# Kernel optimization log

Measured on AMD Instinct MI355X. Metric: run time of the kernel, lower is better.

The kernel has to match this reference:

```python
import jax, jax.numpy as jnp
import numpy as np

B, L, E, D, H, P, NL = 4, 2048, 7, 512, 8, 720, 2
DH = D // H
FACTOR = 5
U = min(L, FACTOR * int(np.ceil(np.log(L))))  # top-u queries, = 40
SCALE = 1.0 / np.sqrt(DH)


def setup_inputs() -> dict:
    key = jax.random.key(0)
    ks = jax.random.split(key, 12)
    s = 0.02
    rn = lambda k, shape: jax.random.normal(k, shape, jnp.float32) * s
    return {
        "x": jax.random.normal(ks[0], (B, L, E), jnp.float32),
        "emb_w": rn(ks[1], (E, D)), "emb_b": jnp.zeros((D,), jnp.float32),
        "Wq": rn(ks[2], (NL, D, D)), "bq": jnp.zeros((NL, D), jnp.float32),
        "Wk": rn(ks[3], (NL, D, D)), "bk": jnp.zeros((NL, D), jnp.float32),
        "Wv": rn(ks[4], (NL, D, D)), "bv": jnp.zeros((NL, D), jnp.float32),
        "Wo": rn(ks[5], (NL, D, D)), "bo": jnp.zeros((NL, D), jnp.float32),
        "W1": rn(ks[6], (NL, D, D)), "b1": jnp.zeros((NL, D), jnp.float32),
        "W2": rn(ks[7], (NL, D, D)), "b2": jnp.zeros((NL, D), jnp.float32),
        "ln1_g": jnp.ones((NL, D), jnp.float32), "ln1_b": jnp.zeros((NL, D), jnp.float32),
        "ln2_g": jnp.ones((NL, D), jnp.float32), "ln2_b": jnp.zeros((NL, D), jnp.float32),
        "proj_w": rn(ks[8], (D, E)), "proj_b": jnp.zeros((E,), jnp.float32),
    }


def layer_norm(x, g, b):
    m = jnp.mean(x, axis=-1, keepdims=True)
    v = jnp.mean(jnp.square(x - m), axis=-1, keepdims=True)
    return (x - m) * jax.lax.rsqrt(v + 1e-5) * g + b


def prob_sparse_attn(x, Wq, bq, Wk, bk, Wv, bv, Wo, bo):
    # x: [B, L, D] -> heads [B, H, L, DH]
    q = (x @ Wq + bq).reshape(B, L, H, DH).transpose(0, 2, 1, 3)
    k = (x @ Wk + bk).reshape(B, L, H, DH).transpose(0, 2, 1, 3)
    v = (x @ Wv + bv).reshape(B, L, H, DH).transpose(0, 2, 1, 3)
    scores = jnp.einsum('bhqd,bhkd->bhqk', q, k) * SCALE  # [B,H,L,L]
    # sparsity measure M(q) = max_k - mean_k
    M = jnp.max(scores, axis=-1) - jnp.mean(scores, axis=-1)  # [B,H,L]
    _, idx = jax.lax.top_k(M, U)  # [B,H,U] indices of active queries
    s_top = jnp.take_along_axis(scores, idx[..., None], axis=2)  # [B,H,U,L]
    attn = jax.nn.softmax(s_top, axis=-1)
    upd = jnp.einsum('bhul,bhld->bhud', attn, v)  # [B,H,U,DH]
    # lazy queries get the mean of V; active queries get attention output
    ctx = jnp.broadcast_to(jnp.mean(v, axis=2, keepdims=True), v.shape)
    bidx = jnp.arange(B)[:, None, None]
    hidx = jnp.arange(H)[None, :, None]
    ctx = ctx.at[bidx, hidx, idx].set(upd)  # scatter active queries
    out = ctx.transpose(0, 2, 1, 3).reshape(B, L, D)
    return out @ Wo + bo


def reference(x, emb_w, emb_b, Wq, bq, Wk, bk, Wv, bv, Wo, bo,
              W1, b1, W2, b2, ln1_g, ln1_b, ln2_g, ln2_b, proj_w, proj_b):
    h = x @ emb_w + emb_b  # [B,L,D]
    for i in range(NL):
        a = prob_sparse_attn(h, Wq[i], bq[i], Wk[i], bk[i], Wv[i], bv[i], Wo[i], bo[i])
        h = layer_norm(h + a, ln1_g[i], ln1_b[i])
        f = jax.nn.relu(h @ W1[i] + b1[i]) @ W2[i] + b2[i]
        h = layer_norm(h + f, ln2_g[i], ln2_b[i])
    return h[:, -P:, :] @ proj_w + proj_b  # [B,P,E]
```

## Files before the change

### kernel.cpp

```cpp
#include <hip/hip_runtime.h>
#include <hip/hip_bf16.h>
#include <cstdint>
#include <cstddef>

#define BB 4
#define LL 2048
#define EE 7
#define DD 512
#define HH 8
#define DHH 64
#define PP 720
#define NLAYER 2
#define UU 40
#define SCALE 0.125f
#define ROWS (BB*LL)
#define BIGN ((size_t)ROWS*DD)
#define NIN 21
#define FCH 256
#define NCH (LL/FCH)
#define PSTR 264
#define VSTR 136

typedef unsigned short u16;
typedef unsigned long long u64;
typedef __bf16 bf16x8 __attribute__((ext_vector_type(8)));
typedef float  f32x4  __attribute__((ext_vector_type(4)));

__device__ __forceinline__ float bf2f(u16 u){
  union { uint32_t i; float f; } c; c.i = ((uint32_t)u) << 16; return c.f;
}
__device__ __forceinline__ u16 f2b(float f){
  __hip_bfloat16 h = __float2bfloat16(f);
  return *(u16*)&h;
}
__device__ __forceinline__ void gld_lds16(const u16* g, u16* l){
  __builtin_amdgcn_global_load_lds(
      (const __attribute__((address_space(1))) uint32_t*)g,
      (__attribute__((address_space(3))) uint32_t*)l, 16, 0, 0);
}
__device__ __forceinline__ int is_bf16(const void* d15){
  return (*(const uint32_t*)d15 == 0x3F800000u) ? 0 : 1;
}

#define NSMALL 15
struct ConvArgs { const void* src[NSMALL]; int off[NSMALL]; int n[NSMALL]; };
struct WPtrs { const void* p[6]; };

__global__ __launch_bounds__(256) void k_preamble(ConvArgs a, WPtrs wp,
    const void* __restrict__ xraw, const void* __restrict__ d15,
    float* __restrict__ dst, float* __restrict__ zbuf,
    u16* __restrict__ hB, u16* __restrict__ wT){
  int y = blockIdx.y, bx = blockIdx.x, t = threadIdx.x;
  int isbf = is_bf16(d15);
  __shared__ u16 tile[64][65];
  __shared__ float xs[32][EE];
  if (y < NSMALL){
    int i = bx*256 + t;
    if (i >= a.n[y]) return;
    float v;
    if (isbf) v = bf2f(((const u16*)a.src[y])[i]);
    else      v = ((const float*)a.src[y])[i];
    dst[(size_t)a.off[y] + i] = v;
  } else if (y == NSMALL){
    int i = bx*256 + t;
    if (i < NLAYER*4096) zbuf[i] = 0.f;
  } else if (y < 32){
    int flat = (y - 16)*256 + bx;
    if (flat >= 512) return;
    int colgrp = flat & 1;
    int rowbase = (flat >> 1) * 32;
    int dd = colgrp*256 + t;
    if (t < 32*EE){
      int j = t / EE, e = t - j*EE;
      xs[j][e] = isbf ? bf2f(((const u16*)xraw)[(rowbase + j)*EE + e])
                      : ((const float*)xraw)[(rowbase + j)*EE + e];
    }
    float wreg[EE];
    #pragma unroll
    for (int e=0;e<EE;e++)
      wreg[e] = isbf ? bf2f(((const u16*)a.src[1])[e*DD + dd])
                     : ((const float*)a.src[1])[e*DD + dd];
    float bias = isbf ? bf2f(((const u16*)a.src[2])[dd]) : ((const float*)a.src[2])[dd];
    __syncthreads();
    for (int j=0;j<32;j++){
      float acc = bias;
      #pragma unroll
      for (int e=0;e<EE;e++) acc = fmaf(xs[j][e], wreg[e], acc);
      hB[(size_t)(rowbase + j)*DD + dd] = f2b(acc);
    }
  } else {
    int flat = (y - 32)*256 + bx;
    int mz = flat >> 6, tl = flat & 63;
    int lay = mz / 6, mat = mz % 6;
    int n0 = (tl & 7)*64, k0 = (tl >> 3)*64;
    int r = t >> 6, c = t & 63;
    const void* src = wp.p[mat];
    for (int rr = r; rr < 64; rr += 4){
      size_t idx = ((size_t)lay*DD + (k0+rr))*DD + n0 + c;
      u16 v;
      if (isbf) v = ((const u16*)src)[idx];
      else      v = f2b(((const float*)src)[idx]);
      tile[rr][c] = v;
    }
    __syncthreads();
    u16* drow = wT + ((size_t)mz*DD + n0)*DD + k0;
    int c4 = (t & 15)*4;
    for (int rr = (t >> 4); rr < 64; rr += 16){
      ushort4 v = { tile[c4][rr], tile[c4+1][rr], tile[c4+2][rr], tile[c4+3][rr] };
      *(ushort4*)(drow + (size_t)rr*DD + c4) = v;
    }
  }
}

__global__ __launch_bounds__(256) void k_gemm_mfma(const u16* __restrict__ A, const u16* __restrict__ Bt,
    const float* __restrict__ bias, u16* __restrict__ Cb, int relu){
  __shared__ u16 As[64*64];
  __shared__ u16 Bs[128*64];
  int t = threadIdx.x, wave = t >> 6, lane = t & 63;
  int qlane = lane & 15, quad = lane >> 4;
  int flat = blockIdx.x + gridDim.x*blockIdx.y;
  int xcd = flat & 7, rest = flat >> 3;
  int mb = (xcd + 8*(rest & 15)) * 64;
  int nb = (rest >> 4) * 128;
  int wm = (wave & 1) * 32, wn = (wave >> 1) * 64;
  f32x4 acc[2][4];
  #pragma unroll
  for (int i=0;i<2;i++)
    #pragma unroll
    for (int j=0;j<4;j++) acc[i][j] = (f32x4){0.f,0.f,0.f,0.f};

  int srow = wave*8 + (lane>>3);
  int scol = (((lane&7) ^ ((lane>>3)&7))) * 8;
  const u16* Ag = A + (size_t)(mb + srow)*DD + scol;
  const u16* Bg = Bt + (size_t)(nb + srow)*DD + scol;

  for (int k0 = 0; k0 < DD; k0 += 64){
    __syncthreads();
    #pragma unroll
    for (int i=0;i<2;i++)
      gld_lds16(Ag + (size_t)i*32*DD + k0, As + (i*32 + wave*8)*64);
    #pragma unroll
    for (int i=0;i<4;i++)
      gld_lds16(Bg + (size_t)i*32*DD + k0, Bs + (i*32 + wave*8)*64);
    __syncthreads();
    #pragma unroll
    for (int ch=0; ch<2; ++ch){
      bf16x8 af[2], bfv[4];
      int cgL = ((ch*4 + quad) ^ (qlane & 7)) * 8;
      #pragma unroll
      for (int i=0;i<2;i++) af[i] = *(const bf16x8*)(As + (wm + i*16 + qlane)*64 + cgL);
      #pragma unroll
      for (int j=0;j<4;j++) bfv[j] = *(const bf16x8*)(Bs + (wn + j*16 + qlane)*64 + cgL);
      #pragma unroll
      for (int i=0;i<2;i++)
        #pragma unroll
        for (int j=0;j<4;j++)
          acc[i][j] = __builtin_amdgcn_mfma_f32_16x16x32_bf16(af[i], bfv[j], acc[i][j], 0, 0, 0);
    }
  }
  #pragma unroll
  for (int i=0;i<2;i++){
    int rbase = mb + wm + i*16 + quad*4;
    #pragma unroll
    for (int j=0;j<4;j++){
      int col = nb + wn + j*16 + qlane;
      float bv = bias[col];
      #pragma unroll
      for (int r=0;r<4;r++){
        float cv = acc[i][j][r] + bv;
        if (relu) cv = fmaxf(cv, 0.f);
        Cb[(size_t)(rbase + r)*DD + col] = f2b(cv);
      }
    }
  }
}

__global__ __launch_bounds__(256) void k_gemm_wo(const u64* __restrict__ rowPtr, const u16* __restrict__ Bt,
    const float* __restrict__ bias, u16* __restrict__ Cb){
  __shared__ u16 As[64*64];
  __shared__ u16 Bs[128*64];
  int t = threadIdx.x, wave = t >> 6, lane = t & 63;
  int qlane = lane & 15, quad = lane >> 4;
  int flat = blockIdx.x + gridDim.x*blockIdx.y;
  int xcd = flat & 7, rest = flat >> 3;
  int mb = (xcd + 8*(rest & 15)) * 64;
  int nb = (rest >> 4) * 128;
  int wm = (wave & 1) * 32, wn = (wave >> 1) * 64;
  f32x4 acc[2][4];
  #pragma unroll
  for (int i=0;i<2;i++)
    #pragma unroll
    for (int j=0;j<4;j++) acc[i][j] = (f32x4){0.f,0.f,0.f,0.f};

  int srow = wave*8 + (lane>>3);
  int scol = (((lane&7) ^ ((lane>>3)&7))) * 8;
  const u16* Bg = Bt + (size_t)(nb + srow)*DD + scol;

  for (int k0 = 0; k0 < DD; k0 += 64){
    int slice = k0 >> 6;
    __syncthreads();
    #pragma unroll
    for (int i=0;i<2;i++){
      int arow = mb + i*32 + srow;
      const u16* src = (const u16*)(uintptr_t)rowPtr[(size_t)arow*8 + slice] + scol;
      gld_lds16(src, As + (i*32 + wave*8)*64);
    }
    #pragma unroll
    for (int i=0;i<4;i++)
      gld_lds16(Bg + (size_t)i*32*DD + k0, Bs + (i*32 + wave*8)*64);
    __syncthreads();
    #pragma unroll
    for (int ch=0; ch<2; ++ch){
      bf16x8 af[2], bfv[4];
      int cgL = ((ch*4 + quad) ^ (qlane & 7)) * 8;
      #pragma unroll
      for (int i=0;i<2;i++) af[i] = *(const bf16x8*)(As + (wm + i*16 + qlane)*64 + cgL);
      #pragma unroll
      for (int j=0;j<4;j++) bfv[j] = *(const bf16x8*)(Bs + (wn + j*16 + qlane)*64 + cgL);
      #pragma unroll
      for (int i=0;i<2;i++)
        #pragma unroll
        for (int j=0;j<4;j++)
          acc[i][j] = __builtin_amdgcn_mfma_f32_16x16x32_bf16(af[i], bfv[j], acc[i][j], 0, 0, 0);
    }
  }
  #pragma unroll
  for (int i=0;i<2;i++){
    int rbase = mb + wm + i*16 + quad*4;
    #pragma unroll
    for (int j=0;j<4;j++){
      int col = nb + wn + j*16 + qlane;
      float bv = bias[col];
      #pragma unroll
      for (int r=0;r<4;r++){
        float cv = acc[i][j][r] + bv;
        Cb[(size_t)(rbase + r)*DD + col] = f2b(cv);
      }
    }
  }
}

__global__ __launch_bounds__(256) void k_gemm_qkv(const u16* __restrict__ A, const u16* __restrict__ Wt,
    const float* __restrict__ bq, const float* __restrict__ bk, const float* __restrict__ bv,
    u16* __restrict__ qB, u16* __restrict__ kB, u16* __restrict__ vB,
    float* __restrict__ ksum, float* __restrict__ vsum){
  __shared__ u16 As[128*64];
  __shared__ u16 Bs[128*64];
  int t = threadIdx.x, wave = t >> 6, lane = t & 63;
  int qlane = lane & 15, quad = lane >> 4;
  int flat = blockIdx.x + gridDim.x*blockIdx.y;
  int xcd = flat & 7, rest = flat >> 3;
  int mb  = (xcd + 8*(rest & 7)) * 128;
  int nbg = (rest >> 3) * 128;
  int sel = nbg >> 9;
  int nb  = nbg & 511;
  const float* bias = (sel==0) ? bq : (sel==1) ? bk : bv;
  u16* out = (sel==0) ? qB : (sel==1) ? kB : vB;
  const u16* Bt = Wt + (size_t)sel*DD*DD;
  int wm = (wave & 1) * 64, wn = (wave >> 1) * 64;
  f32x4 acc[4][4];
  #pragma unroll
  for (int i=0;i<4;i++)
    #pragma unroll
    for (int j=0;j<4;j++) acc[i][j] = (f32x4){0.f,0.f,0.f,0.f};

  int srow = wave*8 + (lane>>3);
  int scol = (((lane&7) ^ ((lane>>3)&7))) * 8;
  const u16* Ag = A + (size_t)(mb + srow)*DD + scol;
  const u16* Bg = Bt + (size_t)(nb + srow)*DD + scol;

  for (int k0 = 0; k0 < DD; k0 += 64){
    __syncthreads();
    #pragma unroll
    for (int i=0;i<4;i++){
      gld_lds16(Ag + (size_t)i*32*DD + k0, As + (i*32 + wave*8)*64);
      gld_lds16(Bg + (size_t)i*32*DD + k0, Bs + (i*32 + wave*8)*64);
    }
    __syncthreads();
    #pragma unroll
    for (int ch=0; ch<2; ++ch){
      bf16x8 af[4], bf[4];
      int cgL = ((ch*4 + quad) ^ (qlane & 7)) * 8;
      #pragma unroll
      for (int i=0;i<4;i++) af[i] = *(const bf16x8*)(As + (wm + i*16 + qlane)*64 + cgL);
      #pragma unroll
      for (int j=0;j<4;j++) bf[j] = *(const bf16x8*)(Bs + (wn + j*16 + qlane)*64 + cgL);
      #pragma unroll
      for (int i=0;i<4;i++)
        #pragma unroll
        for (int j=0;j<4;j++)
          acc[i][j] = __builtin_amdgcn_mfma_f32_16x16x32_bf16(af[i], bf[j], acc[i][j], 0, 0, 0);
    }
  }
  float csum[4] = {0.f,0.f,0.f,0.f};
  #pragma unroll
  for (int j=0;j<4;j++){
    int col = nb + wn + j*16 + qlane;
    float bvv = bias[col];
    #pragma unroll
    for (int i=0;i<4;i++){
      int rbase = mb + wm + i*16 + quad*4;
      #pragma unroll
      for (int r=0;r<4;r++){
        float cv = acc[i][j][r] + bvv;
        out[(size_t)(rbase + r)*DD + col] = f2b(cv);
        csum[j] += cv;
      }
    }
  }
  if (sel > 0){
    float* dst = (sel==1) ? ksum : vsum;
    int bidx = mb >> 11;
    #pragma unroll
    for (int j=0;j<4;j++){
      float v = csum[j];
      v += __shfl_xor(v, 16);
      v += __shfl_xor(v, 32);
      if ((lane>>4) == 0)
        atomicAdd(dst + bidx*512 + nb + wn + j*16 + lane, v);
    }
  }
}

__global__ __launch_bounds__(256) void k_sparsity_mfma(const u16* __restrict__ qB, const u16* __restrict__ kB,
    const float* __restrict__ ksum, float* __restrict__ Mout){
  int flat = blockIdx.x + gridDim.x*blockIdx.y;
  int xcd = flat & 7, rest = flat >> 3;
  int qc = rest & 15;
  int bh = (rest >> 4)*8 + xcd;
  int b = bh >> 3, hh = bh & 7;
  int q0 = qc * 128;
  int t = threadIdx.x, wave = t >> 6, lane = t & 63;
  const u16* qbase = qB + ((size_t)(b*LL + q0))*DD + hh*DHH;
  const u16* kbase = kB + ((size_t)b*LL)*DD + hh*DHH;
  bf16x8 qa[8][2];
  #pragma unroll
  for (int i=0;i<8;i++)
    #pragma unroll
    for (int c=0;c<2;c++)
      qa[i][c] = *(const bf16x8*)(qbase + (size_t)(i*16 + (lane&15))*DD + c*32 + (lane>>4)*8);
  float rmax[8][4];
  #pragma unroll
  for (int i=0;i<8;i++)
    #pragma unroll
    for (int r=0;r<4;r++) rmax[i][r] = -3.0e38f;
  for (int kt = wave*16; kt < LL; kt += 64){
    bf16x8 kb0 = *(const bf16x8*)(kbase + (size_t)(kt + (lane&15))*DD + (lane>>4)*8);
    bf16x8 kb1 = *(const bf16x8*)(kbase + (size_t)(kt + (lane&15))*DD + 32 + (lane>>4)*8);
    #pragma unroll
    for (int i=0;i<8;i++){
      f32x4 a = (f32x4){0.f,0.f,0.f,0.f};
      a = __builtin_amdgcn_mfma_f32_16x16x32_bf16(qa[i][0], kb0, a, 0, 0, 0);
      a = __builtin_amdgcn_mfma_f32_16x16x32_bf16(qa[i][1], kb1, a, 0, 0, 0);
      #pragma unroll
      for (int r=0;r<4;r++) rmax[i][r] = fmaxf(rmax[i][r], a[r]);
    }
  }
  #pragma unroll
  for (int i=0;i<8;i++)
    #pragma unroll
    for (int r=0;r<4;r++){
      float v = rmax[i][r];
      v = fmaxf(v, __shfl_xor(v, 1));
      v = fmaxf(v, __shfl_xor(v, 2));
      v = fmaxf(v, __shfl_xor(v, 4));
      v = fmaxf(v, __shfl_xor(v, 8));
      rmax[i][r] = v;
    }
  __shared__ float smax[4][128];
  if ((lane & 15) == 0){
    #pragma unroll
    for (int i=0;i<8;i++)
      #pragma unroll
      for (int r=0;r<4;r++)
        smax[wave][i*16 + (lane>>4)*4 + r] = rmax[i][r];
  }
  __syncthreads();
  if (t < 128){
    float mx = fmaxf(fmaxf(smax[0][t], smax[1][t]), fmaxf(smax[2][t], smax[3][t]));
    const u16* qrow = qB + (size_t)(b*LL + q0 + t)*DD + hh*DHH;
    float dot = 0.f;
    #pragma unroll
    for (int dv=0; dv<16; ++dv){
      ushort4 qv = *(const ushort4*)(qrow + dv*4);
      const float* kp = ksum + bh*DHH + dv*4;
      dot += bf2f(qv.x)*kp[0] + bf2f(qv.y)*kp[1]
           + bf2f(qv.z)*kp[2] + bf2f(qv.w)*kp[3];
    }
    Mout[bh*LL + q0 + t] = SCALE * (mx - dot * (1.0f/LL));
  }
}

__global__ __launch_bounds__(256) void k_flash(const u16* __restrict__ qB, const u16* __restrict__ kB,
    const u16* __restrict__ vB, const float* __restrict__ Mv, int* __restrict__ sidx,
    float* __restrict__ pO, float* __restrict__ pM, float* __restrict__ pS){
  int bh = blockIdx.y, c = blockIdx.x;
  int b = bh >> 3, hh = bh & 7;
  int t = threadIdx.x, w = t >> 6, lane = t & 63;
  int qlane = lane & 15, quad = lane >> 4;
  int l0 = c * FCH;
  __shared__ u16 Ps[48*PSTR];
  __shared__ union { uint32_t keys[LL]; u16 vst[64*VSTR]; } uu;
  __shared__ float wred[4][48];
  __shared__ float mrow[48];
  __shared__ int hist[256];
  __shared__ int scr[2];
  __shared__ int tieIdx[64];
  __shared__ int counters[2];
  __shared__ int sidxL[UU], sidxS[UU];

  {
    const float* src = Mv + (size_t)bh*LL;
    #pragma unroll
    for (int j = 0; j < 8; ++j){
      int idx = t + j*256;
      uint32_t u = __float_as_uint(src[idx]);
      uu.keys[idx] = (u & 0x80000000u) ? ~u : (u | 0x80000000u);
    }
    uint32_t prefix = 0, pmask = 0;
    int need = UU;
    #pragma unroll
    for (int pass = 0; pass < 4; ++pass){
      int shift = 24 - pass*8;
      __syncthreads();
      hist[t] = 0;
      __syncthreads();
      #pragma unroll
      for (int j = 0; j < 8; ++j){
        uint32_t k = uu.keys[t + j*256];
        if ((k & pmask) == prefix)
          atomicAdd(&hist[(k >> shift) & 0xFF], 1);
      }
      __syncthreads();
      if (t < 64){
        int ln = t;
        int h0 = hist[ln*4+0], h1 = hist[ln*4+1], h2 = hist[ln*4+2], h3 = hist[ln*4+3];
        int s = h0 + h1 + h2 + h3;
        int acc = s;
        #pragma unroll
        for (int off = 1; off < 64; off <<= 1){
          int v = __shfl_down(acc, off);
          if (ln + off < 64) acc += v;
        }
        int c3 = acc - s;
        int c2 = c3 + h3;
        int c1 = c2 + h2;
        int c0 = c1 + h1;
        if      (need > c3 && need <= c3 + h3){ scr[0] = ln*4+3; scr[1] = c3; }
        else if (need > c2 && need <= c2 + h2){ scr[0] = ln*4+2; scr[1] = c2; }
        else if (need > c1 && need <= c1 + h1){ scr[0] = ln*4+1; scr[1] = c1; }
        else if (need > c0 && need <= c0 + h0){ scr[0] = ln*4+0; scr[1] = c0; }
      }
      __syncthreads();
      prefix |= ((uint32_t)scr[0]) << shift;
      need -= scr[1];
      pmask |= 0xFFu << shift;
    }
    if (t < 2) counters[t] = 0;
    __syncthreads();
    uint32_t Tkey = prefix;
    #pragma unroll
    for (int j = 0; j < 8; ++j){
      int idx = t + j*256;
      uint32_t k = uu.keys[idx];
      if (k > Tkey){
        int p = atomicAdd(&counters[0], 1);
        sidxL[p] = idx;
      } else if (k == Tkey){
        int p = atomicAdd(&counters[1], 1);
        if (p < 64) tieIdx[p] = idx;
      }
    }
    __syncthreads();
    if (t == 0){
      int c_gt = counters[0];
      int tc = counters[1];
      int needTies = UU - c_gt;
      if (tc <= 64){
        for (int m = 0; m < needTies; ++m){
          int bestv = 0x7FFFFFFF, bestp = -1;
          for (int q = 0; q < tc; ++q)
            if (tieIdx[q] < bestv){ bestv = tieIdx[q]; bestp = q; }
          sidxL[c_gt + m] = bestv;
          tieIdx[bestp] = 0x7FFFFFFF;
        }
      } else {
        int m = 0;
        for (int j = 0; j < LL && m < needTies; ++j)
          if (uu.keys[j] == Tkey){ sidxL[c_gt + m] = j; m++; }
      }
    }
    __syncthreads();
    int vv = 0, rk = 0;
    if (t < UU){
      vv = sidxL[t];
      #pragma unroll 8
      for (int j = 0; j < UU; ++j) rk += (sidxL[j] < vv) ? 1 : 0;
    }
    __syncthreads();
    if (t < UU) sidxS[rk] = vv;
    __syncthreads();
    if (c == 0 && t < UU) sidx[bh*UU + t] = sidxS[t];
  }

  const u16* kbase = kB + (size_t)b*LL*DD + hh*DHH;
  const u16* vbase = vB + (size_t)b*LL*DD + hh*DHH;
  const u16* qbase = qB + (size_t)b*LL*DD + hh*DHH;

  bf16x8 qa[3][2];
  #pragma unroll
  for (int i=0;i<3;i++){
    int u = i*16 + qlane;
    if (u < UU){
      const u16* qr = qbase + (size_t)sidxS[u]*DD + quad*8;
      qa[i][0] = *(const bf16x8*)qr;
      qa[i][1] = *(const bf16x8*)(qr + 32);
    } else {
      bf16x8 z;
      #pragma unroll
      for (int q8=0;q8<8;q8++) z[q8] = (__bf16)0.0f;
      qa[i][0] = z; qa[i][1] = z;
    }
  }
  f32x4 S[3][4];
  #pragma unroll
  for (int j=0;j<4;j++){
    const u16* kr = kbase + (size_t)(l0 + w*64 + j*16 + qlane)*DD + quad*8;
    bf16x8 k0 = *(const bf16x8*)kr;
    bf16x8 k1 = *(const bf16x8*)(kr + 32);
    #pragma unroll
    for (int i=0;i<3;i++){
      f32x4 a = (f32x4){0.f,0.f,0.f,0.f};
      a = __builtin_amdgcn_mfma_f32_16x16x32_bf16(qa[i][0], k0, a, 0, 0, 0);
      a = __builtin_amdgcn_mfma_f32_16x16x32_bf16(qa[i][1], k1, a, 0, 0, 0);
      S[i][j] = a;
    }
  }
  #pragma unroll
  for (int i=0;i<3;i++){
    #pragma unroll
    for (int r=0;r<4;r++){
      float m = -3.0e38f;
      #pragma unroll
      for (int j=0;j<4;j++){ S[i][j][r] *= SCALE; m = fmaxf(m, S[i][j][r]); }
      m = fmaxf(m, __shfl_xor(m, 1));
      m = fmaxf(m, __shfl_xor(m, 2));
      m = fmaxf(m, __shfl_xor(m, 4));
      m = fmaxf(m, __shfl_xor(m, 8));
      if (qlane == 0) wred[w][i*16 + quad*4 + r] = m;
    }
  }
  __syncthreads();
  if (t < 48) mrow[t] = fmaxf(fmaxf(wred[0][t], wred[1][t]), fmaxf(wred[2][t], wred[3][t]));
  __syncthreads();
  #pragma unroll
  for (int i=0;i<3;i++){
    #pragma unroll
    for (int r=0;r<4;r++){
      int row = i*16 + quad*4 + r;
      float m = mrow[row];
      float ls = 0.f;
      #pragma unroll
      for (int j=0;j<4;j++){
        float e = __expf(S[i][j][r] - m);
        ls += e;
        Ps[row*PSTR + w*64 + j*16 + qlane] = f2b(e);
      }
      ls += __shfl_xor(ls, 1);
      ls += __shfl_xor(ls, 2);
      ls += __shfl_xor(ls, 4);
      ls += __shfl_xor(ls, 8);
      if (qlane == 0) wred[w][row] = ls;
    }
  }
  __syncthreads();
  if (t < 48){
    pM[(bh*NCH + c)*48 + t] = mrow[t];
    pS[(bh*NCH + c)*48 + t] = wred[0][t] + wred[1][t] + wred[2][t] + wred[3][t];
  }
  f32x4 O[3];
  #pragma unroll
  for (int i=0;i<3;i++) O[i] = (f32x4){0.f,0.f,0.f,0.f};
  for (int half = 0; half < 2; ++half){
    __syncthreads();
    for (int idx = t; idx < 128*64; idx += 256){
      int rr = idx >> 6, d = idx & 63;
      uu.vst[d*VSTR + rr] = vbase[(size_t)(l0 + half*128 + rr)*DD + d];
    }
    __syncthreads();
    #pragma unroll
    for (int ks = 0; ks < 4; ++ks){
      int kloc = half*128 + ks*32;
      bf16x8 bfv = *(const bf16x8*)(uu.vst + (w*16 + qlane)*VSTR + ks*32 + quad*8);
      #pragma unroll
      for (int i=0;i<3;i++){
        bf16x8 af = *(const bf16x8*)(Ps + (i*16 + qlane)*PSTR + kloc + quad*8);
        O[i] = __builtin_amdgcn_mfma_f32_16x16x32_bf16(af, bfv, O[i], 0, 0, 0);
      }
    }
  }
  size_t ob = (size_t)(bh*NCH + c)*48*64;
  #pragma unroll
  for (int i=0;i<3;i++)
    #pragma unroll
    for (int r=0;r<4;r++)
      pO[ob + (size_t)(i*16 + quad*4 + r)*64 + w*16 + qlane] = O[i][r];
}

__global__ __launch_bounds__(256) void k_flash_red(const float* __restrict__ pO, const float* __restrict__ pM,
    const float* __restrict__ pS, const int* __restrict__ sidx, const float* __restrict__ vsum,
    u16* __restrict__ attnC, u16* __restrict__ vmeanB, u64* __restrict__ rowPtr){
  int bh = blockIdx.x; int b = bh >> 3, hh = bh & 7;
  int t = threadIdx.x;
  if (t < 64) vmeanB[b*512 + hh*64 + t] = f2b(vsum[b*512 + hh*64 + t] * (1.0f/LL));
  u64 vmPtr = (u64)(uintptr_t)(vmeanB + b*512 + hh*64);
  for (int row = t; row < LL; row += 256)
    rowPtr[((size_t)b*LL + row)*8 + hh] = vmPtr;
  __syncthreads();
  if (t < UU)
    rowPtr[((size_t)b*LL + sidx[bh*UU + t])*8 + hh] =
        (u64)(uintptr_t)(attnC + ((size_t)bh*UU + t)*64);
  for (int idx = t; idx < UU*64; idx += 256){
    int u = idx >> 6, n = idx & 63;
    float m = -3.0e38f;
    #pragma unroll
    for (int c=0;c<NCH;c++) m = fmaxf(m, pM[(bh*NCH + c)*48 + u]);
    float s = 0.f, o = 0.f;
    #pragma unroll
    for (int c=0;c<NCH;c++){
      float wgt = __expf(pM[(bh*NCH + c)*48 + u] - m);
      s += wgt * pS[(bh*NCH + c)*48 + u];
      o += wgt * pO[((size_t)(bh*NCH + c)*48 + u)*64 + n];
    }
    attnC[((size_t)bh*UU + u)*64 + n] = f2b(o / s);
  }
}

__global__ __launch_bounds__(256) void k_addln(const u16* __restrict__ a, const u16* __restrict__ r,
    const float* __restrict__ g, const float* __restrict__ bvec, u16* __restrict__ outB){
  int row = blockIdx.x*4 + (threadIdx.x >> 6);
  int lane = threadIdx.x & 63;
  size_t base = (size_t)row * DD + lane*8;
  ushort4 a0 = *(const ushort4*)(a + base);
  ushort4 a1 = *(const ushort4*)(a + base + 4);
  ushort4 r0 = *(const ushort4*)(r + base);
  ushort4 r1 = *(const ushort4*)(r + base + 4);
  float x[8] = {bf2f(a0.x)+bf2f(r0.x), bf2f(a0.y)+bf2f(r0.y),
                bf2f(a0.z)+bf2f(r0.z), bf2f(a0.w)+bf2f(r0.w),
                bf2f(a1.x)+bf2f(r1.x), bf2f(a1.y)+bf2f(r1.y),
                bf2f(a1.z)+bf2f(r1.z), bf2f(a1.w)+bf2f(r1.w)};
  float s = 0.f;
  #pragma unroll
  for (int i=0;i<8;i++) s += x[i];
  #pragma unroll
  for (int off=1; off<64; off<<=1) s += __shfl_xor(s, off);
  float mean = s * (1.0f/DD);
  float vs = 0.f;
  #pragma unroll
  for (int i=0;i<8;i++){ x[i] -= mean; vs += x[i]*x[i]; }
  #pragma unroll
  for (int off=1; off<64; off<<=1) vs += __shfl_xor(vs, off);
  float rs = rsqrtf(vs * (1.0f/DD) + 1e-5f);
  const float* gp = g + lane*8;
  const float* bp = bvec + lane*8;
  u16 ob[8];
  #pragma unroll
  for (int i=0;i<8;i++) ob[i] = f2b(x[i]*rs*gp[i] + bp[i]);
  *(ushort4*)(outB + base)     = (ushort4){ob[0],ob[1],ob[2],ob[3]};
  *(ushort4*)(outB + base + 4) = (ushort4){ob[4],ob[5],ob[6],ob[7]};
}

__global__ __launch_bounds__(256) void k_proj(const u16* __restrict__ hB, const float* __restrict__ pw,
    const float* __restrict__ pb, void* __restrict__ out, const void* __restrict__ d15){
  int rp = blockIdx.x*4 + (threadIdx.x >> 6);
  int lane = threadIdx.x & 63;
  int b = rp / PP, pp = rp - b*PP;
  const u16* hr = hB + (size_t)(b*LL + (LL-PP) + pp) * DD + lane*8;
  ushort4 v0 = *(const ushort4*)hr;
  ushort4 v1 = *(const ushort4*)(hr + 4);
  float x[8] = {bf2f(v0.x), bf2f(v0.y), bf2f(v0.z), bf2f(v0.w),
                bf2f(v1.x), bf2f(v1.y), bf2f(v1.z), bf2f(v1.w)};
  float acc[EE];
  #pragma unroll
  for (int e=0;e<EE;e++) acc[e]=0.f;
  #pragma unroll
  for (int j=0;j<8;j++){
    const float* wrow = pw + (size_t)(lane*8 + j)*EE;
    #pragma unroll
    for (int e=0;e<EE;e++) acc[e] = fmaf(x[j], wrow[e], acc[e]);
  }
  int isbf = is_bf16(d15);
  #pragma unroll
  for (int e=0;e<EE;e++){
    float rr = acc[e];
    #pragma unroll
    for (int off=32; off>0; off>>=1) rr += __shfl_down(rr, off);
    if (lane == 0){
      float val = rr + pb[e];
      if (isbf) ((__hip_bfloat16*)out)[(size_t)rp*EE + e] = __float2bfloat16(val);
      else      ((float*)out)[(size_t)rp*EE + e] = val;
    }
  }
}

extern "C" void kernel_launch(void* const* d_in, const int* in_sizes, int n_in,
                              void* d_out, int out_size, void* d_ws, size_t ws_size,
                              hipStream_t stream){
  float* ws    = (float*)d_ws;
  float* Mv    = ws;
  float* ksumL = Mv + (size_t)BB*HH*LL;
  float* pM    = ksumL + NLAYER*4096;
  float* pS    = pM + 12288;
  float* pO    = pS + 12288;
  int*   sidx  = (int*)(pO + 786432);
  u64*   rowPtr= (u64*)(((uintptr_t)(sidx + 1280) + 15) & ~(uintptr_t)15);
  u16*   attnC = (u16*)(rowPtr + (size_t)ROWS*8);
  u16*   vmeanB= attnC + (size_t)BB*HH*UU*64;
  u16*   hB    = vmeanB + 2048;
  u16*   qB    = hB + BIGN;
  u16*   kB    = qB + BIGN;
  u16*   vB    = kB + BIGN;
  u16*   f1B   = vB + BIGN;
  u16*   tmpB  = f1B + BIGN;
  u16*   wT    = tmpB + BIGN;
  float* conv  = (float*)(((uintptr_t)(wT + (size_t)12*DD*DD) + 15) & ~(uintptr_t)15);

  static const int small_ids[NSMALL] = {0,1,2,4,6,8,10,12,14,15,16,17,18,19,20};
  ConvArgs ca;
  int off_all[NIN];
  int tot = 0;
  for (int i = 0; i < NIN; ++i) off_all[i] = -1;
  for (int s = 0; s < NSMALL; ++s){
    int i = small_ids[s];
    ca.src[s] = d_in[i];
    ca.off[s] = tot;
    ca.n[s]   = in_sizes[i];
    off_all[i] = tot;
    tot += in_sizes[i];
  }
  const float* bq = conv + off_all[4];
  const float* bk = conv + off_all[6];
  const float* bv = conv + off_all[8];
  const float* bo = conv + off_all[10];
  const float* b1 = conv + off_all[12];
  const float* b2 = conv + off_all[14];
  const float* ln1g = conv + off_all[15]; const float* ln1b = conv + off_all[16];
  const float* ln2g = conv + off_all[17]; const float* ln2b = conv + off_all[18];
  const float* pw = conv + off_all[19]; const float* pb = conv + off_all[20];

  WPtrs wp;
  wp.p[0]=d_in[3]; wp.p[1]=d_in[5]; wp.p[2]=d_in[7];
  wp.p[3]=d_in[9]; wp.p[4]=d_in[11]; wp.p[5]=d_in[13];

  k_preamble<<<dim3(256, 35), 256, 0, stream>>>(ca, wp, d_in[0], d_in[15],
                                                conv, ksumL, hB, wT);

  dim3 gg(4, 128);
  dim3 gq(3*DD/128, ROWS/128);

  for (int l = 0; l < NLAYER; ++l){
    const u16* WqkvT = wT + (size_t)(l*6 + 0)*DD*DD;
    const u16* WoT   = wT + (size_t)(l*6 + 3)*DD*DD;
    const u16* W1T   = wT + (size_t)(l*6 + 4)*DD*DD;
    const u16* W2T   = wT + (size_t)(l*6 + 5)*DD*DD;
    float* ksum = ksumL + l*4096;
    float* vsum = ksum + 2048;

    k_gemm_qkv<<<gq, 256, 0, stream>>>(hB, WqkvT, bq + l*DD, bk + l*DD, bv + l*DD,
                                       qB, kB, vB, ksum, vsum);
    k_sparsity_mfma<<<dim3(LL/128, BB*HH), 256, 0, stream>>>(qB, kB, ksum, Mv);
    k_flash<<<dim3(NCH, BB*HH), 256, 0, stream>>>(qB, kB, vB, Mv, sidx, pO, pM, pS);
    k_flash_red<<<BB*HH, 256, 0, stream>>>(pO, pM, pS, sidx, vsum, attnC, vmeanB, rowPtr);
    k_gemm_wo<<<gg, 256, 0, stream>>>(rowPtr, WoT, bo + l*DD, tmpB);
    k_addln<<<ROWS/4, 256, 0, stream>>>(hB, tmpB, ln1g + l*DD, ln1b + l*DD, hB);
    k_gemm_mfma<<<gg, 256, 0, stream>>>(hB, W1T, b1 + l*DD, f1B, 1);
    k_gemm_mfma<<<gg, 256, 0, stream>>>(f1B, W2T, b2 + l*DD, tmpB, 0);
    k_addln<<<ROWS/4, 256, 0, stream>>>(hB, tmpB, ln2g + l*DD, ln2b + l*DD, hB);
  }
  k_proj<<<(BB*PP)/4, 256, 0, stream>>>(hB, pw, pb, d_out, d_in[15]);
}
```

Before: 362.3 us.

## Restrict last-layer post-attention work to output window and fuse final LN into projection

In the final layer, the Wo GEMM, first add+LayerNorm and both FFN GEMMs now run only on a 768-row window per batch (offset 1280), covering the last 720 rows actually projected, instead of all 2048. The final add+LayerNorm is fused into the projection kernel, so the full hidden state is not written back and reread. Tile mapping gains per-batch window parameters. This removes unneeded row work and one launch; the risk is mapping errors, since the window is sized to 12 tiles of 64 and must cover the tail rows exactly.

```diff
diff --git a/kernel.cpp b/kernel.cpp
--- a/kernel.cpp
+++ b/kernel.cpp
@@ -20,6 +20,9 @@
 #define NCH (LL/FCH)
 #define PSTR 264
 #define VSTR 136
+#define WOFF 1280
+#define WTPB 12
+#define WRPB 768
 
 typedef unsigned short u16;
 typedef unsigned long long u64;
@@ -40,6 +43,45 @@
 }
 __device__ __forceinline__ int is_bf16(const void* d15){
   return (*(const uint32_t*)d15 == 0x3F800000u) ? 0 : 1;
+}
+
+__device__ __forceinline__ void addln_row_vals(const u16* a, const u16* r,
+    const float* g, const float* bvec, int row, int lane, u16 ob[8]){
+  size_t base = (size_t)row * DD + lane*8;
+  ushort4 a0 = *(const ushort4*)(a + base);
+  ushort4 a1 = *(const ushort4*)(a + base + 4);
+  ushort4 r0 = *(const ushort4*)(r + base);
+  ushort4 r1 = *(const ushort4*)(r + base + 4);
+  float x[8] = {bf2f(a0.x)+bf2f(r0.x), bf2f(a0.y)+bf2f(r0.y),
+                bf2f(a0.z)+bf2f(r0.z), bf2f(a0.w)+bf2f(r0.w),
+                bf2f(a1.x)+bf2f(r1.x), bf2f(a1.y)+bf2f(r1.y),
+                bf2f(a1.z)+bf2f(r1.z), bf2f(a1.w)+bf2f(r1.w)};
+  float s = 0.f;
+  #pragma unroll
+  for (int i=0;i<8;i++) s += x[i];
+  #pragma unroll
+  for (int off=1; off<64; off<<=1) s += __shfl_xor(s, off);
+  float mean = s * (1.0f/DD);
+  float vs = 0.f;
+  #pragma unroll
+  for (int i=0;i<8;i++){ x[i] -= mean; vs += x[i]*x[i]; }
+  #pragma unroll
+  for (int off=1; off<64; off<<=1) vs += __shfl_xor(vs, off);
+  float rs = rsqrtf(vs * (1.0f/DD) + 1e-5f);
+  const float* gp = g + lane*8;
+  const float* bp = bvec + lane*8;
+  #pragma unroll
+  for (int i=0;i<8;i++) ob[i] = f2b(x[i]*rs*gp[i] + bp[i]);
+}
+
+__device__ __forceinline__ void tile_map(int flat, int tilesPerB, int winOff,
+                                         int* mbRow, int* nbOut){
+  int mq = tilesPerB >> 1;
+  int xcd = flat & 7, rest = flat >> 3;
+  int mbi = xcd + 8*(rest % mq);
+  int bat = mbi / tilesPerB;
+  *mbRow = bat*LL + winOff + (mbi - bat*tilesPerB)*64;
+  *nbOut = (rest / mq) * 128;
 }
 
 #define NSMALL 15
@@ -113,15 +155,15 @@
 }
 
 __global__ __launch_bounds__(256) void k_gemm_mfma(const u16* __restrict__ A, const u16* __restrict__ Bt,
-    const float* __restrict__ bias, u16* __restrict__ Cb, int relu){
+    const float* __restrict__ bias, u16* __restrict__ Cb, int relu,
+    int tilesPerB, int winOff){
   __shared__ u16 As[64*64];
   __shared__ u16 Bs[128*64];
   int t = threadIdx.x, wave = t >> 6, lane = t & 63;
   int qlane = lane & 15, quad = lane >> 4;
   int flat = blockIdx.x + gridDim.x*blockIdx.y;
-  int xcd = flat & 7, rest = flat >> 3;
-  int mb = (xcd + 8*(rest & 15)) * 64;
-  int nb = (rest >> 4) * 128;
+  int mb, nb;
+  tile_map(flat, tilesPerB, winOff, &mb, &nb);
   int wm = (wave & 1) * 32, wn = (wave >> 1) * 64;
   f32x4 acc[2][4];
   #pragma unroll
@@ -176,15 +218,15 @@
 }
 
 __global__ __launch_bounds__(256) void k_gemm_wo(const u64* __restrict__ rowPtr, const u16* __restrict__ Bt,
-    const float* __restrict__ bias, u16* __restrict__ Cb){
+    const float* __restrict__ bias, u16* __restrict__ Cb,
+    int tilesPerB, int winOff){
   __shared__ u16 As[64*64];
   __shared__ u16 Bs[128*64];
   int t = threadIdx.x, wave = t >> 6, lane = t & 63;
   int qlane = lane & 15, quad = lane >> 4;
   int flat = blockIdx.x + gridDim.x*blockIdx.y;
-  int xcd = flat & 7, rest = flat >> 3;
-  int mb = (xcd + 8*(rest & 15)) * 64;
-  int nb = (rest >> 4) * 128;
+  int mb, nb;
+  tile_map(flat, tilesPerB, winOff, &mb, &nb);
   int wm = (wave & 1) * 32, wn = (wave >> 1) * 64;
   f32x4 acc[2][4];
   #pragma unroll
@@ -637,49 +679,32 @@
 }
 
 __global__ __launch_bounds__(256) void k_addln(const u16* __restrict__ a, const u16* __restrict__ r,
-    const float* __restrict__ g, const float* __restrict__ bvec, u16* __restrict__ outB){
-  int row = blockIdx.x*4 + (threadIdx.x >> 6);
+    const float* __restrict__ g, const float* __restrict__ bvec, u16* __restrict__ outB,
+    int rowsPerB, int winOff){
+  int g0 = blockIdx.x*4 + (threadIdx.x >> 6);
   int lane = threadIdx.x & 63;
+  int bat = g0 / rowsPerB;
+  int row = bat*LL + winOff + (g0 - bat*rowsPerB);
+  u16 ob[8];
+  addln_row_vals(a, r, g, bvec, row, lane, ob);
   size_t base = (size_t)row * DD + lane*8;
-  ushort4 a0 = *(const ushort4*)(a + base);
-  ushort4 a1 = *(const ushort4*)(a + base + 4);
-  ushort4 r0 = *(const ushort4*)(r + base);
-  ushort4 r1 = *(const ushort4*)(r + base + 4);
-  float x[8] = {bf2f(a0.x)+bf2f(r0.x), bf2f(a0.y)+bf2f(r0.y),
-                bf2f(a0.z)+bf2f(r0.z), bf2f(a0.w)+bf2f(r0.w),
-                bf2f(a1.x)+bf2f(r1.x), bf2f(a1.y)+bf2f(r1.y),
-                bf2f(a1.z)+bf2f(r1.z), bf2f(a1.w)+bf2f(r1.w)};
-  float s = 0.f;
-  #pragma unroll
-  for (int i=0;i<8;i++) s += x[i];
-  #pragma unroll
-  for (int off=1; off<64; off<<=1) s += __shfl_xor(s, off);
-  float mean = s * (1.0f/DD);
-  float vs = 0.f;
-  #pragma unroll
-  for (int i=0;i<8;i++){ x[i] -= mean; vs += x[i]*x[i]; }
-  #pragma unroll
-  for (int off=1; off<64; off<<=1) vs += __shfl_xor(vs, off);
-  float rs = rsqrtf(vs * (1.0f/DD) + 1e-5f);
-  const float* gp = g + lane*8;
-  const float* bp = bvec + lane*8;
-  u16 ob[8];
-  #pragma unroll
-  for (int i=0;i<8;i++) ob[i] = f2b(x[i]*rs*gp[i] + bp[i]);
   *(ushort4*)(outB + base)     = (ushort4){ob[0],ob[1],ob[2],ob[3]};
   *(ushort4*)(outB + base + 4) = (ushort4){ob[4],ob[5],ob[6],ob[7]};
 }
 
-__global__ __launch_bounds__(256) void k_proj(const u16* __restrict__ hB, const float* __restrict__ pw,
-    const float* __restrict__ pb, void* __restrict__ out, const void* __restrict__ d15){
-  int rp = blockIdx.x*4 + (threadIdx.x >> 6);
-  int lane = threadIdx.x & 63;
+__global__ __launch_bounds__(256) void k_proj_ln(const u16* __restrict__ hIn, const u16* __restrict__ res,
+    const float* __restrict__ lng, const float* __restrict__ lnbv,
+    const float* __restrict__ pw, const float* __restrict__ pb,
+    void* __restrict__ out, const void* __restrict__ d15){
+  int w = threadIdx.x >> 6, lane = threadIdx.x & 63;
+  int rp = blockIdx.x*4 + w;
   int b = rp / PP, pp = rp - b*PP;
-  const u16* hr = hB + (size_t)(b*LL + (LL-PP) + pp) * DD + lane*8;
-  ushort4 v0 = *(const ushort4*)hr;
-  ushort4 v1 = *(const ushort4*)(hr + 4);
-  float x[8] = {bf2f(v0.x), bf2f(v0.y), bf2f(v0.z), bf2f(v0.w),
-                bf2f(v1.x), bf2f(v1.y), bf2f(v1.z), bf2f(v1.w)};
+  int row = b*LL + (LL-PP) + pp;
+  u16 ob[8];
+  addln_row_vals(hIn, res, lng, lnbv, row, lane, ob);
+  float x[8];
+  #pragma unroll
+  for (int j=0;j<8;j++) x[j] = bf2f(ob[j]);
   float acc[EE];
   #pragma unroll
   for (int e=0;e<EE;e++) acc[e]=0.f;
@@ -755,7 +780,8 @@
   k_preamble<<<dim3(256, 35), 256, 0, stream>>>(ca, wp, d_in[0], d_in[15],
                                                 conv, ksumL, hB, wT);
 
-  dim3 gg(4, 128);
+  dim3 gg0(4, 128);
+  dim3 gg1(4, WTPB*BB);
   dim3 gq(3*DD/128, ROWS/128);
 
   for (int l = 0; l < NLAYER; ++l){
@@ -771,11 +797,20 @@
     k_sparsity_mfma<<<dim3(LL/128, BB*HH), 256, 0, stream>>>(qB, kB, ksum, Mv);
     k_flash<<<dim3(NCH, BB*HH), 256, 0, stream>>>(qB, kB, vB, Mv, sidx, pO, pM, pS);
     k_flash_red<<<BB*HH, 256, 0, stream>>>(pO, pM, pS, sidx, vsum, attnC, vmeanB, rowPtr);
-    k_gemm_wo<<<gg, 256, 0, stream>>>(rowPtr, WoT, bo + l*DD, tmpB);
-    k_addln<<<ROWS/4, 256, 0, stream>>>(hB, tmpB, ln1g + l*DD, ln1b + l*DD, hB);
-    k_gemm_mfma<<<gg, 256, 0, stream>>>(hB, W1T, b1 + l*DD, f1B, 1);
-    k_gemm_mfma<<<gg, 256, 0, stream>>>(f1B, W2T, b2 + l*DD, tmpB, 0);
-    k_addln<<<ROWS/4, 256, 0, stream>>>(hB, tmpB, ln2g + l*DD, ln2b + l*DD, hB);
-  }
-  k_proj<<<(BB*PP)/4, 256, 0, stream>>>(hB, pw, pb, d_out, d_in[15]);
-}
+    if (l < NLAYER - 1){
+      k_gemm_wo<<<gg0, 256, 0, stream>>>(rowPtr, WoT, bo + l*DD, tmpB, 32, 0);
+      k_addln<<<ROWS/4, 256, 0, stream>>>(hB, tmpB, ln1g + l*DD, ln1b + l*DD, hB, LL, 0);
+      k_gemm_mfma<<<gg0, 256, 0, stream>>>(hB, W1T, b1 + l*DD, f1B, 1, 32, 0);
+      k_gemm_mfma<<<gg0, 256, 0, stream>>>(f1B, W2T, b2 + l*DD, tmpB, 0, 32, 0);
+      k_addln<<<ROWS/4, 256, 0, stream>>>(hB, tmpB, ln2g + l*DD, ln2b + l*DD, hB, LL, 0);
+    } else {
+      k_gemm_wo<<<gg1, 256, 0, stream>>>(rowPtr, WoT, bo + l*DD, tmpB, WTPB, WOFF);
+      k_addln<<<(WRPB*BB)/4, 256, 0, stream>>>(hB, tmpB, ln1g + l*DD, ln1b + l*DD, hB,
+                                               WRPB, WOFF);
+      k_gemm_mfma<<<gg1, 256, 0, stream>>>(hB, W1T, b1 + l*DD, f1B, 1, WTPB, WOFF);
+      k_gemm_mfma<<<gg1, 256, 0, stream>>>(f1B, W2T, b2 + l*DD, tmpB, 0, WTPB, WOFF);
+      k_proj_ln<<<(BB*PP)/4, 256, 0, stream>>>(hB, tmpB, ln2g + l*DD, ln2b + l*DD,
+                                               pw, pb, d_out, d_in[15]);
+    }
+  }
+}
```

After: 348.2 us. -3.9%, faster.
